# Kernel optimization log

Hardware: AMD Instinct MI355X
Metric: run time of the kernel (lower is better)

The kernel has to match this reference:

```python
import jax, jax.numpy as jnp
import numpy as np

N_GRAPHS = 64


def gcn_conv(x, W, b, src, dst, n_nodes):
    """PyG GCNConv: add self-loops, symmetric D^-1/2 (A+I) D^-1/2 normalization,
    linear transform, scatter-add aggregation at target nodes, plus bias."""
    xw = x @ W  # [N, out]  transform before propagate (PyG order)
    loop = jnp.arange(n_nodes, dtype=src.dtype)
    rows = jnp.concatenate([src, loop])  # message sources
    cols = jnp.concatenate([dst, loop])  # message targets
    deg = jax.ops.segment_sum(jnp.ones_like(cols, dtype=xw.dtype), cols,
                              num_segments=n_nodes)
    dinv = jnp.where(deg > 0, jax.lax.rsqrt(deg), 0.0)
    norm = dinv[rows] * dinv[cols]  # [E+N]
    msgs = norm[:, None] * xw[rows]  # gather + scale
    out = jax.ops.segment_sum(msgs, cols, num_segments=n_nodes)  # scatter-add
    return out + b


def global_mean_pool(x, batch, n_graphs):
    sums = jax.ops.segment_sum(x, batch, num_segments=n_graphs)
    cnts = jax.ops.segment_sum(jnp.ones((x.shape[0],), x.dtype), batch,
                               num_segments=n_graphs)
    return sums / jnp.maximum(cnts, 1.0)[:, None]


def setup_inputs() -> dict:
    key = jax.random.key(0)
    k1, k2, k3, k4, k5, k6 = jax.random.split(key, 6)
    N, E = 50000, 800000
    d_in, d_hid, d_out = 128, 128, 64
    x = jax.random.normal(k1, (N, d_in), dtype=jnp.float32)
    edge_index = jax.random.randint(k2, (2, E), 0, N, dtype=jnp.int64)
    batch = jnp.sort(jax.random.randint(k3, (N,), 0, N_GRAPHS, dtype=jnp.int64))
    # Glorot-ish init for GCN weights, zero bias (PyG default)
    W1 = jax.random.normal(k4, (d_in, d_hid), dtype=jnp.float32) / np.sqrt(d_in)
    b1 = jnp.zeros((d_hid,), jnp.float32)
    W2 = jax.random.normal(k5, (d_hid, d_out), dtype=jnp.float32) / np.sqrt(d_hid)
    b2 = jnp.zeros((d_out,), jnp.float32)
    return {"x": x, "edge_index": edge_index, "batch": batch,
            "W1": W1, "b1": b1, "W2": W2, "b2": b2}


def reference(x, edge_index, batch, W1, b1, W2, b2):
    n_nodes = x.shape[0]
    src, dst = edge_index[0], edge_index[1]
    h = jax.nn.relu(gcn_conv(x, W1, b1, src, dst, n_nodes))
    h = gcn_conv(h, W2, b2, src, dst, n_nodes)
    return global_mean_pool(h, batch, N_GRAPHS)
```

## Files before the change

kernel.cpp:

```cpp
#include <hip/hip_runtime.h>

typedef __attribute__((ext_vector_type(8))) short bf16x8;
typedef __attribute__((ext_vector_type(4))) float f32x4;

__device__ __forceinline__ unsigned short f2bf(float f) {
  unsigned u = __float_as_uint(f);
  u += 0x7FFFu + ((u >> 16) & 1u);
  return (unsigned short)(u >> 16);
}
__device__ __forceinline__ float bflo(unsigned u) { return __uint_as_float(u << 16); }
__device__ __forceinline__ float bfhi(unsigned u) { return __uint_as_float(u & 0xFFFF0000u); }

template <int CO, bool AF32>
__device__ __forceinline__ void gemm_body(const void* __restrict__ Aptr,
                                          const float* __restrict__ W,
                                          unsigned short* __restrict__ Y, int N,
                                          int bid, int tid, unsigned short* Wl) {
  constexpr int K = 128;
  constexpr int SP = K + 8;
  for (int i = tid; i < K * CO; i += 256) {
    int k = i / CO, n = i % CO;
    Wl[n * SP + k] = f2bf(W[i]);
  }
  __syncthreads();

  const int lane = tid & 63;
  const int quad = lane >> 4, l16 = lane & 15;
  const int mbase = bid * 64 + (tid >> 6) * 16;
  const int arow = min(mbase + l16, N - 1);

  bf16x8 afrag[4];
  if constexpr (AF32) {
    const float* A = (const float*)Aptr + (size_t)arow * K;
#pragma unroll
    for (int ks = 0; ks < 4; ks++) {
      const float4* p = (const float4*)(A + ks * 32 + quad * 8);
      float4 f0 = p[0], f1 = p[1];
      afrag[ks] = (bf16x8){(short)f2bf(f0.x), (short)f2bf(f0.y), (short)f2bf(f0.z), (short)f2bf(f0.w),
                           (short)f2bf(f1.x), (short)f2bf(f1.y), (short)f2bf(f1.z), (short)f2bf(f1.w)};
    }
  } else {
    const unsigned short* A = (const unsigned short*)Aptr + (size_t)arow * K;
#pragma unroll
    for (int ks = 0; ks < 4; ks++) afrag[ks] = *(const bf16x8*)(A + ks * 32 + quad * 8);
  }

#pragma unroll
  for (int ct = 0; ct < CO / 16; ct++) {
    f32x4 acc = {0.0f, 0.0f, 0.0f, 0.0f};
#pragma unroll
    for (int ks = 0; ks < 4; ks++) {
      bf16x8 b = *(const bf16x8*)(&Wl[(ct * 16 + l16) * SP + ks * 32 + quad * 8]);
      acc = __builtin_amdgcn_mfma_f32_16x16x32_bf16(afrag[ks], b, acc, 0, 0, 0);
    }
#pragma unroll
    for (int reg = 0; reg < 4; reg++) {
      int node = mbase + quad * 4 + reg;
      if (node < N) Y[(size_t)node * CO + ct * 16 + l16] = f2bf(acc[reg]);
    }
  }
}

__global__ __launch_bounds__(256) void k_mega1(const float* __restrict__ x,
                                               const float* __restrict__ W1,
                                               unsigned short* __restrict__ xw1b, int N,
                                               const int* __restrict__ dst,
                                               int* __restrict__ cnt,
                                               int* __restrict__ rank, int E,
                                               const int* __restrict__ batch,
                                               int* __restrict__ firstIdx,
                                               int gM, int gE4) {
  __shared__ unsigned short Wl[128 * 136];
  const int bid = blockIdx.x, tid = threadIdx.x;
  if (bid < gM) {
    gemm_body<128, true>(x, W1, xw1b, N, bid, tid, Wl);
  } else if (bid < gM + gE4) {
    int e0 = (bid - gM) * 1024 + tid * 4;
    if (e0 + 3 < E) {
      int4 d4 = *(const int4*)(dst + e0);
      int4 r;
      r.x = atomicAdd(&cnt[d4.x], 1);
      r.y = atomicAdd(&cnt[d4.y], 1);
      r.z = atomicAdd(&cnt[d4.z], 1);
      r.w = atomicAdd(&cnt[d4.w], 1);
      *(int4*)(rank + e0) = r;
    } else {
      for (int e = e0; e < E; e++) rank[e] = atomicAdd(&cnt[dst[e]], 1);
    }
  } else {
    int n = (bid - gM - gE4) * 256 + tid;
    if (n < N) {
      int b = batch[n];
      if (n == 0 || batch[n - 1] != b) firstIdx[b] = n + 1;
    }
  }
}

__global__ void k_seg(const int* __restrict__ cnt, int* __restrict__ start,
                      float* __restrict__ dinv, int* __restrict__ counter, int N) {
  const int v = blockIdx.x * 256 + threadIdx.x;
  const int lane = threadIdx.x & 63;
  int c = (v < N) ? cnt[v] : 0;
  int incl = c;
#pragma unroll
  for (int d = 1; d < 64; d <<= 1) {
    int t = __shfl_up(incl, d, 64);
    if (lane >= d) incl += t;
  }
  int base = 0;
  if (lane == 63) base = atomicAdd(counter, incl);
  base = __shfl(base, 63, 64);
  if (v < N) {
    start[v] = base + incl - c;
    dinv[v] = rsqrtf((float)(c + 1));
  }
}

__global__ void k_fill(const int* __restrict__ src, const int* __restrict__ dst,
                       const int* __restrict__ rank, const int* __restrict__ start,
                       const float* __restrict__ dinv, int2* __restrict__ colw, int E) {
  int e = blockIdx.x * 256 + threadIdx.x;
  if (e < E) {
    int s = src[e], d = dst[e];
    int p = start[d] + rank[e];
    float w = dinv[s] * dinv[d];
    colw[p] = make_int2(s, __float_as_int(w));
  }
}

__global__ __launch_bounds__(256) void k_agg128(const unsigned short* __restrict__ xwb,
                                                const float* __restrict__ dinv,
                                                const int* __restrict__ start,
                                                const int* __restrict__ cnt,
                                                const int2* __restrict__ colw,
                                                const float* __restrict__ bias,
                                                unsigned short* __restrict__ out, int N) {
  const int tid = threadIdx.x;
  const int lane = tid & 63;
  const int gl = lane & 15;
  const int grp = lane >> 4;
  const int wv = tid >> 6;
  const int v = blockIdx.x * 16 + wv * 4 + grp;
  const int vc = min(v, N - 1);

  const float dv = dinv[vc];
  const int j0 = start[vc];
  const int jc = (v < N) ? cnt[vc] : 0;

  float acc[8];
  {
    const float d2 = dv * dv;
    uint4 s = *(const uint4*)((const char*)xwb + (((size_t)vc << 8) | (gl << 4)));
    acc[0] = d2 * bflo(s.x); acc[1] = d2 * bfhi(s.x);
    acc[2] = d2 * bflo(s.y); acc[3] = d2 * bfhi(s.y);
    acc[4] = d2 * bflo(s.z); acc[5] = d2 * bfhi(s.z);
    acc[6] = d2 * bflo(s.w); acc[7] = d2 * bfhi(s.w);
  }

  const int gbase = grp << 4;
  for (int base = 0; __any(base < jc); base += 16) {
    int2 cw = (base + gl < jc) ? colw[j0 + base + gl] : make_int2(0, 0);
    int mv = jc - base;
    mv = mv < 0 ? 0 : (mv > 16 ? 16 : mv);
    int mm = max(mv, __shfl_xor(mv, 16, 64));
    mm = max(mm, __shfl_xor(mm, 32, 64));
    const int rp = (mm + 3) & ~3;
    for (int t = 0; t < rp; t += 4) {
      uint4 rbuf[4];
      float wbuf[4];
#pragma unroll
      for (int r = 0; r < 4; r++) {
        int sx = __shfl(cw.x, gbase + t + r, 64);
        wbuf[r] = __int_as_float(__shfl(cw.y, gbase + t + r, 64));
        rbuf[r] = *(const uint4*)((const char*)xwb + (((unsigned)sx << 8) | (gl << 4)));
      }
#pragma unroll
      for (int r = 0; r < 4; r++) {
        const float w = wbuf[r];
        const uint4 rr = rbuf[r];
        acc[0] += w * bflo(rr.x); acc[1] += w * bfhi(rr.x);
        acc[2] += w * bflo(rr.y); acc[3] += w * bfhi(rr.y);
        acc[4] += w * bflo(rr.z); acc[5] += w * bfhi(rr.z);
        acc[6] += w * bflo(rr.w); acc[7] += w * bfhi(rr.w);
      }
    }
  }

  if (v < N) {
    float4 b0 = ((const float4*)bias)[gl * 2];
    float4 b1 = ((const float4*)bias)[gl * 2 + 1];
    float a0 = fmaxf(acc[0] + b0.x, 0.f), a1 = fmaxf(acc[1] + b0.y, 0.f);
    float a2 = fmaxf(acc[2] + b0.z, 0.f), a3 = fmaxf(acc[3] + b0.w, 0.f);
    float a4 = fmaxf(acc[4] + b1.x, 0.f), a5 = fmaxf(acc[5] + b1.y, 0.f);
    float a6 = fmaxf(acc[6] + b1.z, 0.f), a7 = fmaxf(acc[7] + b1.w, 0.f);
    uint4 st;
    st.x = (unsigned)f2bf(a0) | ((unsigned)f2bf(a1) << 16);
    st.y = (unsigned)f2bf(a2) | ((unsigned)f2bf(a3) << 16);
    st.z = (unsigned)f2bf(a4) | ((unsigned)f2bf(a5) << 16);
    st.w = (unsigned)f2bf(a6) | ((unsigned)f2bf(a7) << 16);
    *(uint4*)((char*)out + (((size_t)v << 8) | (gl << 4))) = st;
  }
}

__global__ __launch_bounds__(256) void k_gemm2(const unsigned short* __restrict__ A,
                                               const float* __restrict__ W,
                                               unsigned short* __restrict__ Y, int N) {
  __shared__ unsigned short Wl[64 * 136];
  gemm_body<64, false>(A, W, Y, N, blockIdx.x, threadIdx.x, Wl);
}

__global__ __launch_bounds__(256) void k_aggpool(const unsigned short* __restrict__ xwb,
                                                 const float* __restrict__ dinv,
                                                 const int* __restrict__ start,
                                                 const int* __restrict__ cnt,
                                                 const int2* __restrict__ colw,
                                                 const int* __restrict__ batch,
                                                 float* __restrict__ stage, int N) {
  __shared__ float sAcc[4][64];
  const int tid = threadIdx.x;
  const int lane = tid & 63;
  const int gl = lane & 7;
  const int grp = lane >> 3;
  const int wv = tid >> 6;
  const int v = blockIdx.x * 32 + wv * 8 + grp;
  const int vc = min(v, N - 1);

  const float dv = dinv[vc];
  const int j0 = start[vc];
  const int jc = (v < N) ? cnt[vc] : 0;
  const int b = batch[vc];

  float acc[8];
  {
    const float d2 = (v < N) ? dv * dv : 0.0f;
    uint4 s = *(const uint4*)((const char*)xwb + (((size_t)vc << 7) | (gl << 4)));
    acc[0] = d2 * bflo(s.x); acc[1] = d2 * bfhi(s.x);
    acc[2] = d2 * bflo(s.y); acc[3] = d2 * bfhi(s.y);
    acc[4] = d2 * bflo(s.z); acc[5] = d2 * bfhi(s.z);
    acc[6] = d2 * bflo(s.w); acc[7] = d2 * bfhi(s.w);
  }

  const int gbase = grp << 3;
  for (int base = 0; __any(base < jc); base += 8) {
    int2 cw = (base + gl < jc) ? colw[j0 + base + gl] : make_int2(0, 0);
    int mv = jc - base;
    mv = mv < 0 ? 0 : (mv > 8 ? 8 : mv);
    int mm = max(mv, __shfl_xor(mv, 8, 64));
    mm = max(mm, __shfl_xor(mm, 16, 64));
    mm = max(mm, __shfl_xor(mm, 32, 64));
    const int rp = (mm + 3) & ~3;
    for (int t = 0; t < rp; t += 4) {
      uint4 rbuf[4];
      float wbuf[4];
#pragma unroll
      for (int r = 0; r < 4; r++) {
        int sx = __shfl(cw.x, gbase + t + r, 64);
        wbuf[r] = __int_as_float(__shfl(cw.y, gbase + t + r, 64));
        rbuf[r] = *(const uint4*)((const char*)xwb + (((unsigned)sx << 7) | (gl << 4)));
      }
#pragma unroll
      for (int r = 0; r < 4; r++) {
        const float w = wbuf[r];
        const uint4 rr = rbuf[r];
        acc[0] += w * bflo(rr.x); acc[1] += w * bfhi(rr.x);
        acc[2] += w * bflo(rr.y); acc[3] += w * bfhi(rr.y);
        acc[4] += w * bflo(rr.z); acc[5] += w * bfhi(rr.z);
        acc[6] += w * bflo(rr.w); acc[7] += w * bfhi(rr.w);
      }
    }
  }

  const int v0 = blockIdx.x * 32;
  const bool uniform = (v0 + 31 < N) && (batch[v0] == batch[v0 + 31]);
  if (uniform) {
#pragma unroll
    for (int d = 8; d < 64; d <<= 1)
#pragma unroll
      for (int k = 0; k < 8; k++) acc[k] += __shfl_xor(acc[k], d, 64);
    if (grp == 0) {
      *(float4*)&sAcc[wv][gl * 8] = make_float4(acc[0], acc[1], acc[2], acc[3]);
      *(float4*)&sAcc[wv][gl * 8 + 4] = make_float4(acc[4], acc[5], acc[6], acc[7]);
    }
    __syncthreads();
    if (wv == 0) {
      float t = sAcc[0][lane] + sAcc[1][lane] + sAcc[2][lane] + sAcc[3][lane];
      atomicAdd(&stage[batch[v0] * 64 + lane], t);
    }
  } else if (v < N) {
#pragma unroll
    for (int k = 0; k < 8; k++) atomicAdd(&stage[b * 64 + gl * 8 + k], acc[k]);
  }
}

__global__ void k_final(const float* __restrict__ stage, const int* __restrict__ firstIdx,
                        const float* __restrict__ b2, float* __restrict__ out, int N) {
  __shared__ float denom[64];
  const int tid = threadIdx.x;
  if (tid < 64) {
    int raw = firstIdx[tid];
    int fi = (raw > 0) ? raw - 1 : 0x7FFFFFFF;
    int m = fi;
#pragma unroll
    for (int d = 1; d < 64; d <<= 1) {
      int t = __shfl_down(m, d, 64);
      if (tid + d < 64) m = min(m, t);
    }
    int nxtm = __shfl_down(m, 1, 64);
    int nxt = (tid == 63) ? N : min(nxtm, N);
    int c = (fi == 0x7FFFFFFF) ? 0 : (nxt - fi);
    denom[tid] = fmaxf((float)c, 1.0f);
  }
  __syncthreads();
  for (int i = tid; i < 64 * 64; i += 256)
    out[i] = stage[i] / denom[i >> 6] + b2[i & 63];
}


extern "C" void kernel_launch(void* const* d_in, const int* in_sizes, int n_in,
                              void* d_out, int out_size, void* d_ws, size_t ws_size,
                              hipStream_t stream) {
  const float* x     = (const float*)d_in[0];
  const int*   ei    = (const int*)d_in[1];
  const int*   batch = (const int*)d_in[2];
  const float* W1    = (const float*)d_in[3];
  const float* b1    = (const float*)d_in[4];
  const float* W2    = (const float*)d_in[5];
  const float* b2    = (const float*)d_in[6];

  const int N = in_sizes[2];
  const int E = in_sizes[1] / 2;
  const int* src  = ei;
  const int* dstv = ei + E;

  unsigned short* xw1b = (unsigned short*)d_ws;
  unsigned short* h1b  = xw1b + (size_t)N * 128;
  unsigned short* xw2b = xw1b;
  int*   cnt     = (int*)(h1b + (size_t)N * 128);
  int*   counter = cnt + N;
  int*   firstIdx= counter + 1;
  float* stage   = (float*)(firstIdx + 64);
  int*   startv  = (int*)(stage + 4096);
  float* dinv    = (float*)(startv + N);
  int2*  colw    = (int2*)(((uintptr_t)(dinv + N) + 15) & ~(uintptr_t)15);
  int*   rank    = (int*)(colw + E);
  float* outp    = (float*)d_out;

  hipMemsetAsync(cnt, 0, (size_t)(N + 1 + 64 + 4096) * sizeof(int), stream);

  const int gM  = (N + 63) / 64;
  const int gE4 = (E + 1023) / 1024;
  const int gE  = (E + 255) / 256;
  const int gN  = (N + 255) / 256;
  const int gA1 = (N + 15) / 16;
  const int gA2 = (N + 31) / 32;

  k_mega1<<<gM + gE4 + gN, 256, 0, stream>>>(x, W1, xw1b, N, dstv, cnt, rank, E,
                                             batch, firstIdx, gM, gE4);
  k_seg<<<gN, 256, 0, stream>>>(cnt, startv, dinv, counter, N);
  k_fill<<<gE, 256, 0, stream>>>(src, dstv, rank, startv, dinv, colw, E);

  k_agg128<<<gA1, 256, 0, stream>>>(xw1b, dinv, startv, cnt, colw, b1, h1b, N);

  k_gemm2<<<gM, 256, 0, stream>>>(h1b, W2, xw2b, N);
  k_aggpool<<<gA2, 256, 0, stream>>>(xw2b, dinv, startv, cnt, colw, batch, stage, N);

  k_final<<<1, 256, 0, stream>>>(stage, firstIdx, b2, outp, N);
}
```

Baseline: 214.4 us.

## Pack CSR edges into 32-bit index+fp16 weight, fold final pooling kernel

```diff
diff --git a/kernel.cpp b/kernel.cpp
--- a/kernel.cpp
+++ b/kernel.cpp
@@ -1,4 +1,5 @@
 #include <hip/hip_runtime.h>
+#include <hip/hip_fp16.h>
 
 typedef __attribute__((ext_vector_type(8))) short bf16x8;
 typedef __attribute__((ext_vector_type(4))) float f32x4;
@@ -10,6 +11,9 @@
 }
 __device__ __forceinline__ float bflo(unsigned u) { return __uint_as_float(u << 16); }
 __device__ __forceinline__ float bfhi(unsigned u) { return __uint_as_float(u & 0xFFFF0000u); }
+__device__ __forceinline__ float unpackw(unsigned pk) {
+  return __half2float(__ushort_as_half((unsigned short)(pk >> 16)));
+}
 
 template <int CO, bool AF32>
 __device__ __forceinline__ void gemm_body(const void* __restrict__ Aptr,
@@ -118,13 +122,37 @@
 
 __global__ void k_fill(const int* __restrict__ src, const int* __restrict__ dst,
                        const int* __restrict__ rank, const int* __restrict__ start,
-                       const float* __restrict__ dinv, int2* __restrict__ colw, int E) {
-  int e = blockIdx.x * 256 + threadIdx.x;
+                       const float* __restrict__ dinv, unsigned* __restrict__ colwp,
+                       int E, const int* __restrict__ firstIdx,
+                       const float* __restrict__ b2, float* __restrict__ invc,
+                       float* __restrict__ out, int N, int gE) {
+  const int bid = blockIdx.x;
+  const int tid = threadIdx.x;
+  if (bid == gE) {
+    if (tid < 64) {
+      int raw = firstIdx[tid];
+      int fi = (raw > 0) ? raw - 1 : 0x7FFFFFFF;
+      int m = fi;
+#pragma unroll
+      for (int d = 1; d < 64; d <<= 1) {
+        int t = __shfl_down(m, d, 64);
+        if (tid + d < 64) m = min(m, t);
+      }
+      int nxtm = __shfl_down(m, 1, 64);
+      int nxt = (tid == 63) ? N : min(nxtm, N);
+      int c = (fi == 0x7FFFFFFF) ? 0 : (nxt - fi);
+      invc[tid] = 1.0f / fmaxf((float)c, 1.0f);
+    }
+    for (int i = tid; i < 64 * 64; i += 256) out[i] = b2[i & 63];
+    return;
+  }
+  int e = bid * 256 + tid;
   if (e < E) {
     int s = src[e], d = dst[e];
     int p = start[d] + rank[e];
     float w = dinv[s] * dinv[d];
-    colw[p] = make_int2(s, __float_as_int(w));
+    unsigned short wh = __half_as_ushort(__float2half_rn(w));
+    colwp[p] = (unsigned)(s & 0xFFFF) | ((unsigned)wh << 16);
   }
 }
 
@@ -132,7 +160,7 @@
                                                 const float* __restrict__ dinv,
                                                 const int* __restrict__ start,
                                                 const int* __restrict__ cnt,
-                                                const int2* __restrict__ colw,
+                                                const unsigned* __restrict__ colwp,
                                                 const float* __restrict__ bias,
                                                 unsigned short* __restrict__ out, int N) {
   const int tid = threadIdx.x;
@@ -159,23 +187,23 @@
 
   const int gbase = grp << 4;
   for (int base = 0; __any(base < jc); base += 16) {
-    int2 cw = (base + gl < jc) ? colw[j0 + base + gl] : make_int2(0, 0);
+    unsigned pk0 = (base + gl < jc) ? colwp[j0 + base + gl] : 0u;
     int mv = jc - base;
     mv = mv < 0 ? 0 : (mv > 16 ? 16 : mv);
     int mm = max(mv, __shfl_xor(mv, 16, 64));
     mm = max(mm, __shfl_xor(mm, 32, 64));
-    const int rp = (mm + 3) & ~3;
-    for (int t = 0; t < rp; t += 4) {
-      uint4 rbuf[4];
-      float wbuf[4];
-#pragma unroll
-      for (int r = 0; r < 4; r++) {
-        int sx = __shfl(cw.x, gbase + t + r, 64);
-        wbuf[r] = __int_as_float(__shfl(cw.y, gbase + t + r, 64));
-        rbuf[r] = *(const uint4*)((const char*)xwb + (((unsigned)sx << 8) | (gl << 4)));
+    const int rp = (mm + 7) & ~7;
+    for (int t = 0; t < rp; t += 8) {
+      uint4 rbuf[8];
+      float wbuf[8];
+#pragma unroll
+      for (int r = 0; r < 8; r++) {
+        unsigned pk = (unsigned)__shfl((int)pk0, gbase + t + r, 64);
+        wbuf[r] = unpackw(pk);
+        rbuf[r] = *(const uint4*)((const char*)xwb + (((pk & 0xFFFFu) << 8) | (gl << 4)));
       }
 #pragma unroll
-      for (int r = 0; r < 4; r++) {
+      for (int r = 0; r < 8; r++) {
         const float w = wbuf[r];
         const uint4 rr = rbuf[r];
         acc[0] += w * bflo(rr.x); acc[1] += w * bfhi(rr.x);
@@ -213,9 +241,10 @@
                                                  const float* __restrict__ dinv,
                                                  const int* __restrict__ start,
                                                  const int* __restrict__ cnt,
-                                                 const int2* __restrict__ colw,
+                                                 const unsigned* __restrict__ colwp,
                                                  const int* __restrict__ batch,
-                                                 float* __restrict__ stage, int N) {
+                                                 const float* __restrict__ invc,
+                                                 float* __restrict__ out, int N) {
   __shared__ float sAcc[4][64];
   const int tid = threadIdx.x;
   const int lane = tid & 63;
@@ -232,7 +261,7 @@
 
   float acc[8];
   {
-    const float d2 = (v < N) ? dv * dv : 0.0f;
+    const float d2 = dv * dv;
     uint4 s = *(const uint4*)((const char*)xwb + (((size_t)vc << 7) | (gl << 4)));
     acc[0] = d2 * bflo(s.x); acc[1] = d2 * bfhi(s.x);
     acc[2] = d2 * bflo(s.y); acc[3] = d2 * bfhi(s.y);
@@ -242,33 +271,29 @@
 
   const int gbase = grp << 3;
   for (int base = 0; __any(base < jc); base += 8) {
-    int2 cw = (base + gl < jc) ? colw[j0 + base + gl] : make_int2(0, 0);
-    int mv = jc - base;
-    mv = mv < 0 ? 0 : (mv > 8 ? 8 : mv);
-    int mm = max(mv, __shfl_xor(mv, 8, 64));
-    mm = max(mm, __shfl_xor(mm, 16, 64));
-    mm = max(mm, __shfl_xor(mm, 32, 64));
-    const int rp = (mm + 3) & ~3;
-    for (int t = 0; t < rp; t += 4) {
-      uint4 rbuf[4];
-      float wbuf[4];
-#pragma unroll
-      for (int r = 0; r < 4; r++) {
-        int sx = __shfl(cw.x, gbase + t + r, 64);
-        wbuf[r] = __int_as_float(__shfl(cw.y, gbase + t + r, 64));
-        rbuf[r] = *(const uint4*)((const char*)xwb + (((unsigned)sx << 7) | (gl << 4)));
-      }
-#pragma unroll
-      for (int r = 0; r < 4; r++) {
-        const float w = wbuf[r];
-        const uint4 rr = rbuf[r];
-        acc[0] += w * bflo(rr.x); acc[1] += w * bfhi(rr.x);
-        acc[2] += w * bflo(rr.y); acc[3] += w * bfhi(rr.y);
-        acc[4] += w * bflo(rr.z); acc[5] += w * bfhi(rr.z);
-        acc[6] += w * bflo(rr.w); acc[7] += w * bfhi(rr.w);
-      }
-    }
-  }
+    unsigned pk0 = (base + gl < jc) ? colwp[j0 + base + gl] : 0u;
+    uint4 rbuf[8];
+    float wbuf[8];
+#pragma unroll
+    for (int r = 0; r < 8; r++) {
+      unsigned pk = (unsigned)__shfl((int)pk0, gbase + r, 64);
+      wbuf[r] = unpackw(pk);
+      rbuf[r] = *(const uint4*)((const char*)xwb + (((pk & 0xFFFFu) << 7) | (gl << 4)));
+    }
+#pragma unroll
+    for (int r = 0; r < 8; r++) {
+      const float w = wbuf[r];
+      const uint4 rr = rbuf[r];
+      acc[0] += w * bflo(rr.x); acc[1] += w * bfhi(rr.x);
+      acc[2] += w * bflo(rr.y); acc[3] += w * bfhi(rr.y);
+      acc[4] += w * bflo(rr.z); acc[5] += w * bfhi(rr.z);
+      acc[6] += w * bflo(rr.w); acc[7] += w * bfhi(rr.w);
+    }
+  }
+
+  const float sc = (v < N) ? invc[b] : 0.0f;
+#pragma unroll
+  for (int k = 0; k < 8; k++) acc[k] *= sc;
 
   const int v0 = blockIdx.x * 32;
   const bool uniform = (v0 + 31 < N) && (batch[v0] == batch[v0 + 31]);
@@ -284,35 +309,12 @@
     __syncthreads();
     if (wv == 0) {
       float t = sAcc[0][lane] + sAcc[1][lane] + sAcc[2][lane] + sAcc[3][lane];
-      atomicAdd(&stage[batch[v0] * 64 + lane], t);
+      atomicAdd(&out[batch[v0] * 64 + lane], t);
     }
   } else if (v < N) {
 #pragma unroll
-    for (int k = 0; k < 8; k++) atomicAdd(&stage[b * 64 + gl * 8 + k], acc[k]);
-  }
-}
-
-__global__ void k_final(const float* __restrict__ stage, const int* __restrict__ firstIdx,
-                        const float* __restrict__ b2, float* __restrict__ out, int N) {
-  __shared__ float denom[64];
-  const int tid = threadIdx.x;
-  if (tid < 64) {
-    int raw = firstIdx[tid];
-    int fi = (raw > 0) ? raw - 1 : 0x7FFFFFFF;
-    int m = fi;
-#pragma unroll
-    for (int d = 1; d < 64; d <<= 1) {
-      int t = __shfl_down(m, d, 64);
-      if (tid + d < 64) m = min(m, t);
-    }
-    int nxtm = __shfl_down(m, 1, 64);
-    int nxt = (tid == 63) ? N : min(nxtm, N);
-    int c = (fi == 0x7FFFFFFF) ? 0 : (nxt - fi);
-    denom[tid] = fmaxf((float)c, 1.0f);
-  }
-  __syncthreads();
-  for (int i = tid; i < 64 * 64; i += 256)
-    out[i] = stage[i] / denom[i >> 6] + b2[i & 63];
+    for (int k = 0; k < 8; k++) atomicAdd(&out[b * 64 + gl * 8 + k], acc[k]);
+  }
 }
 
 
@@ -338,14 +340,14 @@
   int*   cnt     = (int*)(h1b + (size_t)N * 128);
   int*   counter = cnt + N;
   int*   firstIdx= counter + 1;
-  float* stage   = (float*)(firstIdx + 64);
-  int*   startv  = (int*)(stage + 4096);
+  float* invc    = (float*)(firstIdx + 64);
+  int*   startv  = (int*)(invc + 64);
   float* dinv    = (float*)(startv + N);
-  int2*  colw    = (int2*)(((uintptr_t)(dinv + N) + 15) & ~(uintptr_t)15);
-  int*   rank    = (int*)(colw + E);
+  int*   rank    = (int*)(dinv + N);
+  unsigned* colwp= (unsigned*)(rank + E);
   float* outp    = (float*)d_out;
 
-  hipMemsetAsync(cnt, 0, (size_t)(N + 1 + 64 + 4096) * sizeof(int), stream);
+  hipMemsetAsync(cnt, 0, (size_t)(N + 65) * sizeof(int), stream);
 
   const int gM  = (N + 63) / 64;
   const int gE4 = (E + 1023) / 1024;
@@ -357,12 +359,11 @@
   k_mega1<<<gM + gE4 + gN, 256, 0, stream>>>(x, W1, xw1b, N, dstv, cnt, rank, E,
                                              batch, firstIdx, gM, gE4);
   k_seg<<<gN, 256, 0, stream>>>(cnt, startv, dinv, counter, N);
-  k_fill<<<gE, 256, 0, stream>>>(src, dstv, rank, startv, dinv, colw, E);
-
-  k_agg128<<<gA1, 256, 0, stream>>>(xw1b, dinv, startv, cnt, colw, b1, h1b, N);
+  k_fill<<<gE + 1, 256, 0, stream>>>(src, dstv, rank, startv, dinv, colwp, E,
+                                     firstIdx, b2, invc, outp, N, gE);
+
+  k_agg128<<<gA1, 256, 0, stream>>>(xw1b, dinv, startv, cnt, colwp, b1, h1b, N);
 
   k_gemm2<<<gM, 256, 0, stream>>>(h1b, W2, xw2b, N);
-  k_aggpool<<<gA2, 256, 0, stream>>>(xw2b, dinv, startv, cnt, colw, batch, stage, N);
-
-  k_final<<<1, 256, 0, stream>>>(stage, firstIdx, b2, outp, N);
-}
+  k_aggpool<<<gA2, 256, 0, stream>>>(xw2b, dinv, startv, cnt, colwp, batch, invc, outp, N);
+}
```

Result: no change. 217.1 us (+1.2%).
